# Kernel tuning notes

Measured on AMD Instinct MI355X. Metric: run time of the kernel, lower is better.

The kernel has to match this reference:

```python
import jax, jax.numpy as jnp
import numpy as np

L, D, H, B, S, V = 4, 1024, 16, 8, 512, 32000
DK = D // H          # per-head dim = 64; only head 0 is ever used (bug in source)
FF = 4 * D
EPS = 1e-3           # keras BatchNormalization default epsilon


def _bn(x, gamma, beta, mean, var):
    # inference-mode BatchNorm over last axis (keras default)
    return gamma * (x - mean) * jax.lax.rsqrt(var + EPS) + beta


def setup_inputs() -> dict:
    key = jax.random.key(0)
    keys = iter(jax.random.split(key, 40))

    def rn(shape, scale=0.02):
        return jax.random.normal(next(keys), shape, jnp.float32) * scale

    sequence = jax.random.randint(next(keys), (B, S), 0, V, dtype=jnp.int32)

    # standard sinusoidal positional encoding table [S, D]
    pos = np.arange(S)[:, None].astype(np.float32)
    i = np.arange(D)[None, :]
    angle = pos / np.power(10000.0, (2 * (i // 2)) / D).astype(np.float32)
    pes = np.where(i % 2 == 0, np.sin(angle), np.cos(angle)).astype(np.float32)

    return {
        "sequence": sequence,
        "emb": rn((V, D)),
        "pes": jnp.asarray(pes),
        # single-head attention params (head 0 only, per the source bug), stacked over layers
        "wq": rn((L, D, DK)), "bq": jnp.zeros((L, DK)),
        "wk": rn((L, D, DK)), "bk": jnp.zeros((L, DK)),
        "wv": rn((L, D, DK)), "bv": jnp.zeros((L, DK)),
        "wo": rn((L, DK, D)), "bo": jnp.zeros((L, D)),
        "att_gamma": 1.0 + rn((L, D), 0.1), "att_beta": rn((L, D), 0.1),
        "att_mean": rn((L, D), 0.1), "att_var": jnp.ones((L, D)),
        "w1": rn((L, D, FF)), "bff1": jnp.zeros((L, FF)),
        "w2": rn((L, FF, D)), "bff2": jnp.zeros((L, D)),
        "ffn_gamma": 1.0 + rn((L, D), 0.1), "ffn_beta": rn((L, D), 0.1),
        "ffn_mean": rn((L, D), 0.1), "ffn_var": jnp.ones((L, D)),
    }


def reference(sequence, emb, pes, wq, bq, wk, bk, wv, bv, wo, bo,
              att_gamma, att_beta, att_mean, att_var,
              w1, bff1, w2, bff2,
              ffn_gamma, ffn_beta, ffn_mean, ffn_var):
    # embedding + positional bug: only pes[i, 0] (a scalar per position) is added
    x = emb[sequence] + pes[:S, 0:1][None]          # [B, S, D]
    scale = 1.0 / jnp.sqrt(jnp.float32(DK))
    for l in range(L):
        q = x @ wq[l] + bq[l]                       # [B, S, DK]
        k = x @ wk[l] + bk[l]
        v = x @ wv[l] + bv[l]
        score = jnp.einsum('bqd,bkd->bqk', q, k) * scale
        head = jax.nn.softmax(score, axis=-1) @ v   # [B, S, DK]
        att = head @ wo[l] + bo[l]                  # [B, S, D]
        x = _bn(x + att, att_gamma[l], att_beta[l], att_mean[l], att_var[l])
        ffn = jax.nn.relu(x @ w1[l] + bff1[l]) @ w2[l] + bff2[l]
        x = _bn(x + ffn, ffn_gamma[l], ffn_beta[l], ffn_mean[l], ffn_var[l])
    return x
```

## Files before the change

### kernel.cpp

```cpp
#include <hip/hip_runtime.h>
#include <hip/hip_bf16.h>
#include <stdint.h>

#define L_  4
#define D_  1024
#define DK_ 64
#define B_  8
#define S_  512
#define FF_ 4096
#define M_  (B_*S_)
#define EPS_ 1e-3f
#define QKVN_ 256

typedef __bf16 bf16_t;
typedef bf16_t bf16x8 __attribute__((ext_vector_type(8)));
typedef float  f32x4  __attribute__((ext_vector_type(4)));

__device__ __forceinline__ bf16_t f2b(float f) {
    union { float f; uint32_t u; } v; v.f = f;
    uint32_t r = v.u + 0x7fff + ((v.u >> 16) & 1);
    uint16_t h = (uint16_t)(r >> 16);
    bf16_t o; __builtin_memcpy(&o, &h, 2); return o;
}

__device__ __forceinline__ void gl2lds16(const bf16_t* g, bf16_t* l) {
    __builtin_amdgcn_global_load_lds(
        (__attribute__((address_space(1))) void*)g,
        (__attribute__((address_space(3))) void*)l, 16, 0, 0);
}

__global__ void embed_kernel(const int* __restrict__ seq, const float* __restrict__ emb,
                             const float* __restrict__ pes, float* __restrict__ x,
                             bf16_t* __restrict__ xb) {
    int idx = blockIdx.x * 256 + threadIdx.x;
    int md  = idx >> 10;
    int d   = idx & (D_ - 1);
    int s   = md & (S_ - 1);
    float v = emb[(size_t)seq[md] * D_ + d] + pes[s * D_];
    x[idx] = v;
    xb[idx] = f2b(v);
}

__device__ __forceinline__ void tile_tr(const float* __restrict__ src, bf16_t* __restrict__ dst,
                                        int K, int N, int kb, int nb, float (*t)[33]) {
    int k0 = kb * 32, n0 = nb * 32;
    int c = threadIdx.x & 31, r = threadIdx.x >> 5;
    #pragma unroll
    for (int i = 0; i < 4; i++)
        t[r + i * 8][c] = src[(size_t)(k0 + r + i * 8) * N + n0 + c];
    __syncthreads();
    #pragma unroll
    for (int i = 0; i < 4; i++)
        dst[(size_t)(n0 + r + i * 8) * K + k0 + c] = f2b(t[c][r + i * 8]);
}

__global__ void prep_weights(const float* __restrict__ wq, const float* __restrict__ wk,
                             const float* __restrict__ wv, const float* __restrict__ wo,
                             const float* __restrict__ w1, const float* __restrict__ w2,
                             const float* __restrict__ bq, const float* __restrict__ bk,
                             const float* __restrict__ bv,
                             bf16_t* __restrict__ wqkvt, bf16_t* __restrict__ wot,
                             bf16_t* __restrict__ w1t, bf16_t* __restrict__ w2t,
                             float* __restrict__ bqkv) {
    __shared__ float t[32][33];
    int bid = blockIdx.x;
    if (bid < 4096) {
        tile_tr(w1, w1t, D_, FF_, bid & 31, bid >> 5, t);
    } else if (bid < 8192) {
        int rem = bid - 4096;
        tile_tr(w2, w2t, FF_, D_, rem & 127, rem >> 7, t);
    } else if (bid < 8384) {
        int rem = bid - 8192;
        int which = rem >> 6; rem &= 63;
        const float* src = which == 0 ? wq : (which == 1 ? wk : wv);
        tile_tr(src, wqkvt + (size_t)which * 64 * D_, D_, DK_, rem & 31, rem >> 5, t);
    } else if (bid < 8448) {
        int rem = bid - 8384;
        tile_tr(wo, wot, DK_, D_, rem & 1, rem >> 1, t);
    } else if (bid < 8464) {
        int rem = bid - 8448;
        bf16_t* z = wqkvt + (size_t)192 * D_ + rem * 4096;
        for (int i = threadIdx.x; i < 4096; i += 256) z[i] = (bf16_t)0.f;
    } else {
        int n = threadIdx.x;
        float v = 0.f;
        if      (n <  64) v = bq[n];
        else if (n < 128) v = bk[n - 64];
        else if (n < 192) v = bv[n - 128];
        bqkv[n] = v;
    }
}

template<int MODE>
__global__ __launch_bounds__(256)
void gemm_mfma3(const bf16_t* __restrict__ A, const bf16_t* __restrict__ Bt,
                const float* __restrict__ bias, bf16_t* __restrict__ Cb,
                const float* __restrict__ Xin, float* __restrict__ Xf, bf16_t* __restrict__ Xb,
                const float* __restrict__ g, const float* __restrict__ bb,
                const float* __restrict__ mu, const float* __restrict__ var,
                int N, int K, int kChunk, size_t strideZ) {
    __shared__ bf16_t As[128 * 64];
    __shared__ bf16_t Bs[128 * 64];
    const int tid  = threadIdx.x;
    const int w    = tid >> 6, lane = tid & 63;
    const int wm   = w >> 1,   wn   = w & 1;
    const int lm   = lane & 15, quad = lane >> 4;
    const int m0 = blockIdx.y * 128, n0 = blockIdx.x * 128;
    const int kBeg = blockIdx.z * kChunk, kEnd = kBeg + kChunk;
    const int lrow = lane >> 3;
    const int lk   = (lane & 7) ^ lrow;

    f32x4 acc[4][4];
    #pragma unroll
    for (int i = 0; i < 4; i++)
        #pragma unroll
        for (int j = 0; j < 4; j++) acc[i][j] = (f32x4){0.f, 0.f, 0.f, 0.f};

    for (int k0 = kBeg; k0 < kEnd; k0 += 64) {
        #pragma unroll
        for (int i = 0; i < 4; i++) {
            const int r0 = w * 32 + i * 8;
            gl2lds16(A  + (size_t)(m0 + r0 + lrow) * K + k0 + lk * 8, As + r0 * 64);
            gl2lds16(Bt + (size_t)(n0 + r0 + lrow) * K + k0 + lk * 8, Bs + r0 * 64);
        }
        __syncthreads();
        #pragma unroll
        for (int s = 0; s < 2; s++) {
            bf16x8 af[4], bfr[4];
            #pragma unroll
            for (int mi = 0; mi < 4; mi++) {
                const int ra = wm * 64 + mi * 16 + lm;
                af[mi] = *(const bf16x8*)(As + ra * 64 + (((s * 4 + quad) ^ (lm & 7)) * 8));
            }
            #pragma unroll
            for (int ni = 0; ni < 4; ni++) {
                const int rb = wn * 64 + ni * 16 + lm;
                bfr[ni] = *(const bf16x8*)(Bs + rb * 64 + (((s * 4 + quad) ^ (lm & 7)) * 8));
            }
            #pragma unroll
            for (int mi = 0; mi < 4; mi++)
                #pragma unroll
                for (int ni = 0; ni < 4; ni++)
                    acc[mi][ni] = __builtin_amdgcn_mfma_f32_16x16x32_bf16(
                        af[mi], bfr[ni], acc[mi][ni], 0, 0, 0);
        }
        __syncthreads();
    }

    bf16_t* Pz = (MODE == 2) ? Cb + (size_t)blockIdx.z * strideZ : Cb;

    #pragma unroll
    for (int ni = 0; ni < 4; ni++) {
        const int col = n0 + wn * 64 + ni * 16 + lm;
        float bv = 0.f, gv = 0.f, bbv = 0.f, muv = 0.f, rsv = 0.f;
        if (MODE != 2) bv = bias[col];
        if (MODE == 3) {
            gv = g[col]; bbv = bb[col]; muv = mu[col];
            rsv = rsqrtf(var[col] + EPS_);
        }
        #pragma unroll
        for (int mi = 0; mi < 4; mi++) {
            const int rbase = m0 + wm * 64 + mi * 16 + quad * 4;
            #pragma unroll
            for (int r = 0; r < 4; r++) {
                const size_t idx = (size_t)(rbase + r) * N + col;
                float v = acc[mi][ni][r] + bv;
                if (MODE == 1) Cb[idx] = f2b(fmaxf(v, 0.f));
                if (MODE == 2) Pz[idx] = f2b(v);
                if (MODE == 3) {
                    float s = Xin[idx] + v;
                    float o = gv * (s - muv) * rsv + bbv;
                    Xf[idx] = o;
                    Xb[idx] = f2b(o);
                }
            }
        }
    }
}

__global__ void qkv_reduce(const bf16_t* __restrict__ P, const float* __restrict__ bias,
                           bf16_t* __restrict__ dst) {
    int idx = blockIdx.x * 256 + threadIdx.x;
    int n = idx & (QKVN_ - 1);
    float s = bias[n];
    #pragma unroll
    for (int zz = 0; zz < 4; zz++) s += (float)P[(size_t)zz * M_ * QKVN_ + idx];
    dst[idx] = f2b(s);
}

__global__ void score_kernel(const bf16_t* __restrict__ qkv, float* __restrict__ sc, float scale) {
    int b = blockIdx.z;
    int i0 = blockIdx.y * 64, j0 = blockIdx.x * 64;
    const bf16_t* qb = qkv + (size_t)b * S_ * QKVN_;
    const bf16_t* kb = qb + 64;
    __shared__ float Qs[64][65], Ks[64][65];
    const int tid = threadIdx.y * 16 + threadIdx.x;
    #pragma unroll
    for (int t = 0; t < 16; t++) {
        int idx = tid + t * 256;
        int r = idx >> 6, c = idx & 63;
        Qs[r][c] = (float)qb[(size_t)(i0 + r) * QKVN_ + c];
        Ks[r][c] = (float)kb[(size_t)(j0 + r) * QKVN_ + c];
    }
    __syncthreads();
    float acc[4][4] = {};
    #pragma unroll 8
    for (int d = 0; d < DK_; d++) {
        float a[4], bbv[4];
        #pragma unroll
        for (int i = 0; i < 4; i++) a[i]   = Qs[threadIdx.y * 4 + i][d];
        #pragma unroll
        for (int j = 0; j < 4; j++) bbv[j] = Ks[threadIdx.x * 4 + j][d];
        #pragma unroll
        for (int i = 0; i < 4; i++)
            #pragma unroll
            for (int j = 0; j < 4; j++) acc[i][j] = fmaf(a[i], bbv[j], acc[i][j]);
    }
    float* sb = sc + (size_t)b * S_ * S_;
    #pragma unroll
    for (int i = 0; i < 4; i++)
        #pragma unroll
        for (int j = 0; j < 4; j++)
            sb[(size_t)(i0 + threadIdx.y * 4 + i) * S_ + j0 + threadIdx.x * 4 + j] = acc[i][j] * scale;
}

__global__ void softmax_kernel(float* __restrict__ sc) {
    float* p = sc + (size_t)blockIdx.x * S_;
    int tid = threadIdx.x;
    float v0 = p[tid], v1 = p[tid + 256];
    float m = fmaxf(v0, v1);
    #pragma unroll
    for (int off = 32; off > 0; off >>= 1) m = fmaxf(m, __shfl_xor(m, off, 64));
    __shared__ float wmax[4], wsum[4];
    int wid = tid >> 6, lane = tid & 63;
    if (lane == 0) wmax[wid] = m;
    __syncthreads();
    m = fmaxf(fmaxf(wmax[0], wmax[1]), fmaxf(wmax[2], wmax[3]));
    v0 = __expf(v0 - m); v1 = __expf(v1 - m);
    float s = v0 + v1;
    #pragma unroll
    for (int off = 32; off > 0; off >>= 1) s += __shfl_xor(s, off, 64);
    if (lane == 0) wsum[wid] = s;
    __syncthreads();
    float inv = 1.0f / (wsum[0] + wsum[1] + wsum[2] + wsum[3]);
    p[tid] = v0 * inv; p[tid + 256] = v1 * inv;
}

__global__ void pv_kernel(const float* __restrict__ P, const bf16_t* __restrict__ qkv,
                          float* __restrict__ Hp) {
    int b = blockIdx.z, sp = blockIdx.x;
    const float*  Pb = P + (size_t)b * S_ * S_;
    const bf16_t* Vb = qkv + (size_t)b * S_ * QKVN_ + 128;
    float* Hb = Hp + (size_t)sp * M_ * DK_ + (size_t)b * S_ * DK_;
    int m0 = blockIdx.y * 64;
    __shared__ float Ps[16][65], Vs[16][65];
    const int tid = threadIdx.y * 16 + threadIdx.x;
    float acc[4][4] = {};
    for (int k0 = sp * 128; k0 < sp * 128 + 128; k0 += 16) {
        #pragma unroll
        for (int t = 0; t < 4; t++) {
            int idx = tid + t * 256;
            int r = idx >> 4, c = idx & 15;
            Ps[c][r] = Pb[(size_t)(m0 + r) * S_ + k0 + c];
            int br = idx >> 6, bc = idx & 63;
            Vs[br][bc] = (float)Vb[(size_t)(k0 + br) * QKVN_ + bc];
        }
        __syncthreads();
        #pragma unroll
        for (int kk = 0; kk < 16; kk++) {
            float a[4], bbv[4];
            #pragma unroll
            for (int i = 0; i < 4; i++) a[i]   = Ps[kk][threadIdx.y * 4 + i];
            #pragma unroll
            for (int j = 0; j < 4; j++) bbv[j] = Vs[kk][threadIdx.x * 4 + j];
            #pragma unroll
            for (int i = 0; i < 4; i++)
                #pragma unroll
                for (int j = 0; j < 4; j++) acc[i][j] = fmaf(a[i], bbv[j], acc[i][j]);
        }
        __syncthreads();
    }
    #pragma unroll
    for (int i = 0; i < 4; i++)
        #pragma unroll
        for (int j = 0; j < 4; j++)
            Hb[(size_t)(m0 + threadIdx.y * 4 + i) * DK_ + threadIdx.x * 4 + j] = acc[i][j];
}

__global__ void pv_reduce(const float* __restrict__ Hp, bf16_t* __restrict__ hdb) {
    int idx = blockIdx.x * 256 + threadIdx.x;
    float s = Hp[idx] + Hp[(size_t)M_ * DK_ + idx]
            + Hp[2 * (size_t)M_ * DK_ + idx] + Hp[3 * (size_t)M_ * DK_ + idx];
    hdb[idx] = f2b(s);
}

__global__ void bn_residual2(const float* __restrict__ x, const bf16_t* __restrict__ p,
                             const float* __restrict__ bias,
                             const float* __restrict__ g, const float* __restrict__ b,
                             const float* __restrict__ mu, const float* __restrict__ var,
                             float* __restrict__ dst, bf16_t* __restrict__ dstb) {
    int idx = blockIdx.x * 256 + threadIdx.x;
    int d = idx & (D_ - 1);
    float r = bias[d] + (float)p[idx] + (float)p[(size_t)M_ * D_ + idx];
    float s = x[idx] + r;
    float o = g[d] * (s - mu[d]) * rsqrtf(var[d] + EPS_) + b[d];
    dst[idx] = o;
    dstb[idx] = f2b(o);
}

extern "C" void kernel_launch(void* const* d_in, const int* in_sizes, int n_in,
                              void* d_out, int out_size, void* d_ws, size_t ws_size,
                              hipStream_t stream) {
    const int*   seq = (const int*)  d_in[0];
    const float* emb = (const float*)d_in[1];
    const float* pes = (const float*)d_in[2];
    const float* wq  = (const float*)d_in[3];
    const float* bq  = (const float*)d_in[4];
    const float* wk  = (const float*)d_in[5];
    const float* bk  = (const float*)d_in[6];
    const float* wv  = (const float*)d_in[7];
    const float* bv  = (const float*)d_in[8];
    const float* wo  = (const float*)d_in[9];
    const float* bo  = (const float*)d_in[10];
    const float* ag  = (const float*)d_in[11];
    const float* ab  = (const float*)d_in[12];
    const float* am  = (const float*)d_in[13];
    const float* av  = (const float*)d_in[14];
    const float* w1  = (const float*)d_in[15];
    const float* b1  = (const float*)d_in[16];
    const float* w2  = (const float*)d_in[17];
    const float* b2  = (const float*)d_in[18];
    const float* fg  = (const float*)d_in[19];
    const float* fb  = (const float*)d_in[20];
    const float* fm  = (const float*)d_in[21];
    const float* fv  = (const float*)d_in[22];
    float* out = (float*)d_out;

    char* p = (char*)d_ws;
    auto alloc = [&](size_t bytes) { char* q = p; p += (bytes + 255) & ~(size_t)255; return q; };
    float*  X     = (float*) alloc((size_t)M_ * D_ * 4);
    bf16_t* Xb    = (bf16_t*)alloc((size_t)M_ * D_ * 2);
    bf16_t* qkvb  = (bf16_t*)alloc((size_t)M_ * QKVN_ * 2);
    float*  sc    = (float*) alloc((size_t)B_ * S_ * S_ * 4);
    bf16_t* hdb   = (bf16_t*)alloc((size_t)M_ * DK_ * 2);
    bf16_t* hb    = (bf16_t*)alloc((size_t)M_ * FF_ * 2);
    bf16_t* w1t   = (bf16_t*)alloc((size_t)FF_ * D_ * 2);
    bf16_t* w2t   = (bf16_t*)alloc((size_t)D_ * FF_ * 2);
    bf16_t* wqkvt = (bf16_t*)alloc((size_t)QKVN_ * D_ * 2);
    bf16_t* wot   = (bf16_t*)alloc((size_t)D_ * DK_ * 2);
    float*  bqkv  = (float*) alloc(QKVN_ * 4);

    dim3 blk(16, 16);
    embed_kernel<<<M_ * D_ / 256, 256, 0, stream>>>(seq, emb, pes, X, Xb);

    for (int l = 0; l < L_; l++) {
        prep_weights<<<8465, 256, 0, stream>>>(
            wq + (size_t)l * D_ * DK_, wk + (size_t)l * D_ * DK_, wv + (size_t)l * D_ * DK_,
            wo + (size_t)l * DK_ * D_, w1 + (size_t)l * D_ * FF_, w2 + (size_t)l * FF_ * D_,
            bq + l * DK_, bk + l * DK_, bv + l * DK_,
            wqkvt, wot, w1t, w2t, bqkv);

        gemm_mfma3<2><<<dim3(QKVN_ / 128, M_ / 128, 4), 256, 0, stream>>>(
            Xb, wqkvt, nullptr, (bf16_t*)out, nullptr, nullptr, nullptr,
            nullptr, nullptr, nullptr, nullptr, QKVN_, D_, D_ / 4, (size_t)M_ * QKVN_);
        qkv_reduce<<<M_ * QKVN_ / 256, 256, 0, stream>>>((const bf16_t*)out, bqkv, qkvb);

        score_kernel<<<dim3(S_ / 64, S_ / 64, B_), blk, 0, stream>>>(qkvb, sc, 0.125f);
        softmax_kernel<<<B_ * S_, 256, 0, stream>>>(sc);
        pv_kernel<<<dim3(4, S_ / 64, B_), blk, 0, stream>>>(sc, qkvb, (float*)out);
        pv_reduce<<<M_ * DK_ / 256, 256, 0, stream>>>((const float*)out, hdb);

        gemm_mfma3<3><<<dim3(D_ / 128, M_ / 128, 1), 256, 0, stream>>>(
            hdb, wot, bo + l * D_, nullptr, X, X, Xb,
            ag + l * D_, ab + l * D_, am + l * D_, av + l * D_, D_, DK_, DK_, 0);

        gemm_mfma3<1><<<dim3(FF_ / 128, M_ / 128, 1), 256, 0, stream>>>(
            Xb, w1t, b1 + l * FF_, hb, nullptr, nullptr, nullptr,
            nullptr, nullptr, nullptr, nullptr, FF_, D_, D_, 0);

        gemm_mfma3<2><<<dim3(D_ / 128, M_ / 128, 2), 256, 0, stream>>>(
            hb, w2t, nullptr, (bf16_t*)out, nullptr, nullptr, nullptr,
            nullptr, nullptr, nullptr, nullptr, D_, FF_, FF_ / 2, (size_t)M_ * D_);

        bn_residual2<<<M_ * D_ / 256, 256, 0, stream>>>(
            X, (const bf16_t*)out, b2 + l * D_,
            fg + l * D_, fb + l * D_, fm + l * D_, fv + l * D_, X, Xb);
        if (l == L_ - 1)
            hipMemcpyAsync(out, X, (size_t)M_ * D_ * 4, hipMemcpyDeviceToDevice, stream);
    }
}
```

Before: 986.3 us.

## Fuse score, softmax and PV into one MFMA attention kernel

Replaces the four-kernel scalar-FMA attention path (score, softmax, split PV, reduce) with a fused kernel. It computes QK^T with bf16 MFMA, does the softmax in registers with LDS row reductions, and multiplies P by a pre-transposed V from swizzled LDS. A small transpose kernel writes V^T so it can be staged with wide loads. This removes the fp32 score matrix round trip to global memory and several launches. The trade-offs are that probabilities are rounded to bf16 before the PV product, and the grid is only 64 blocks per layer with large LDS use.

```diff
diff --git a/kernel.cpp b/kernel.cpp
--- a/kernel.cpp
+++ b/kernel.cpp
@@ -188,110 +188,173 @@
     dst[idx] = f2b(s);
 }
 
-__global__ void score_kernel(const bf16_t* __restrict__ qkv, float* __restrict__ sc, float scale) {
-    int b = blockIdx.z;
-    int i0 = blockIdx.y * 64, j0 = blockIdx.x * 64;
-    const bf16_t* qb = qkv + (size_t)b * S_ * QKVN_;
-    const bf16_t* kb = qb + 64;
-    __shared__ float Qs[64][65], Ks[64][65];
-    const int tid = threadIdx.y * 16 + threadIdx.x;
-    #pragma unroll
-    for (int t = 0; t < 16; t++) {
-        int idx = tid + t * 256;
-        int r = idx >> 6, c = idx & 63;
-        Qs[r][c] = (float)qb[(size_t)(i0 + r) * QKVN_ + c];
-        Ks[r][c] = (float)kb[(size_t)(j0 + r) * QKVN_ + c];
+__global__ void vt_kernel(const bf16_t* __restrict__ qkv, bf16_t* __restrict__ Vt) {
+    int b = blockIdx.y, k0 = blockIdx.x * 64;
+    const bf16_t* vb = qkv + (size_t)b * S_ * QKVN_ + 128;
+    __shared__ bf16_t t[64][65];
+    int c = threadIdx.x & 63, r4 = threadIdx.x >> 6;
+    #pragma unroll
+    for (int i = 0; i < 16; i++) {
+        int k = i * 4 + r4;
+        t[c][k] = vb[(size_t)(k0 + k) * QKVN_ + c];
     }
     __syncthreads();
-    float acc[4][4] = {};
-    #pragma unroll 8
-    for (int d = 0; d < DK_; d++) {
-        float a[4], bbv[4];
-        #pragma unroll
-        for (int i = 0; i < 4; i++) a[i]   = Qs[threadIdx.y * 4 + i][d];
-        #pragma unroll
-        for (int j = 0; j < 4; j++) bbv[j] = Ks[threadIdx.x * 4 + j][d];
-        #pragma unroll
-        for (int i = 0; i < 4; i++)
-            #pragma unroll
-            for (int j = 0; j < 4; j++) acc[i][j] = fmaf(a[i], bbv[j], acc[i][j]);
-    }
-    float* sb = sc + (size_t)b * S_ * S_;
-    #pragma unroll
-    for (int i = 0; i < 4; i++)
-        #pragma unroll
-        for (int j = 0; j < 4; j++)
-            sb[(size_t)(i0 + threadIdx.y * 4 + i) * S_ + j0 + threadIdx.x * 4 + j] = acc[i][j] * scale;
-}
-
-__global__ void softmax_kernel(float* __restrict__ sc) {
-    float* p = sc + (size_t)blockIdx.x * S_;
-    int tid = threadIdx.x;
-    float v0 = p[tid], v1 = p[tid + 256];
-    float m = fmaxf(v0, v1);
-    #pragma unroll
-    for (int off = 32; off > 0; off >>= 1) m = fmaxf(m, __shfl_xor(m, off, 64));
-    __shared__ float wmax[4], wsum[4];
-    int wid = tid >> 6, lane = tid & 63;
-    if (lane == 0) wmax[wid] = m;
+    #pragma unroll
+    for (int i = 0; i < 16; i++) {
+        int d = i * 4 + r4;
+        Vt[((size_t)b * DK_ + d) * S_ + k0 + c] = t[d][c];
+    }
+}
+
+__global__ __launch_bounds__(256)
+void attn_fused(const bf16_t* __restrict__ qkv, const bf16_t* __restrict__ Vt,
+                bf16_t* __restrict__ hdb) {
+    const int b  = blockIdx.y;
+    const int i0 = blockIdx.x * 64;
+    const bf16_t* qb  = qkv + (size_t)b * S_ * QKVN_;
+    const bf16_t* kb  = qb + 64;
+    const bf16_t* vtb = Vt + (size_t)b * DK_ * S_;
+
+    __shared__ bf16_t Ps[8 * 64 * 64];
+    __shared__ bf16_t Vs[8 * 64 * 64];
+    __shared__ float  rowred[4][64];
+
+    const int tid  = threadIdx.x;
+    const int w    = tid >> 6, lane = tid & 63;
+    const int lm   = lane & 15, quad = lane >> 4;
+    const int lrow = lane >> 3;
+    const int lk   = (lane & 7) ^ lrow;
+
+    #pragma unroll
+    for (int i = 0; i < 16; i++) {
+        const int r0 = w * 16 + (i & 1) * 8;
+        const int kt = i >> 1;
+        gl2lds16(vtb + (size_t)(r0 + lrow) * S_ + kt * 64 + lk * 8,
+                 Vs + kt * 4096 + r0 * 64);
+    }
+
+    f32x4 acc[4][8];
+    #pragma unroll
+    for (int mi = 0; mi < 4; mi++)
+        #pragma unroll
+        for (int ni = 0; ni < 8; ni++) acc[mi][ni] = (f32x4){0.f, 0.f, 0.f, 0.f};
+
+    #pragma unroll
+    for (int s = 0; s < 2; s++) {
+        bf16x8 af[4], bfr[8];
+        #pragma unroll
+        for (int mi = 0; mi < 4; mi++)
+            af[mi] = *(const bf16x8*)(qb + (size_t)(i0 + mi * 16 + lm) * QKVN_ + s * 32 + quad * 8);
+        #pragma unroll
+        for (int ni = 0; ni < 8; ni++)
+            bfr[ni] = *(const bf16x8*)(kb + (size_t)(w * 128 + ni * 16 + lm) * QKVN_ + s * 32 + quad * 8);
+        #pragma unroll
+        for (int mi = 0; mi < 4; mi++)
+            #pragma unroll
+            for (int ni = 0; ni < 8; ni++)
+                acc[mi][ni] = __builtin_amdgcn_mfma_f32_16x16x32_bf16(
+                    af[mi], bfr[ni], acc[mi][ni], 0, 0, 0);
+    }
+    #pragma unroll
+    for (int mi = 0; mi < 4; mi++)
+        #pragma unroll
+        for (int ni = 0; ni < 8; ni++) acc[mi][ni] *= 0.125f;
+
+    float rmax[4][4];
+    #pragma unroll
+    for (int mi = 0; mi < 4; mi++)
+        #pragma unroll
+        for (int r = 0; r < 4; r++) {
+            float m = acc[mi][0][r];
+            #pragma unroll
+            for (int ni = 1; ni < 8; ni++) m = fmaxf(m, acc[mi][ni][r]);
+            #pragma unroll
+            for (int off = 1; off < 16; off <<= 1) m = fmaxf(m, __shfl_xor(m, off, 64));
+            rmax[mi][r] = m;
+        }
+    if (lm == 0) {
+        #pragma unroll
+        for (int mi = 0; mi < 4; mi++)
+            #pragma unroll
+            for (int r = 0; r < 4; r++)
+                rowred[w][mi * 16 + quad * 4 + r] = rmax[mi][r];
+    }
     __syncthreads();
-    m = fmaxf(fmaxf(wmax[0], wmax[1]), fmaxf(wmax[2], wmax[3]));
-    v0 = __expf(v0 - m); v1 = __expf(v1 - m);
-    float s = v0 + v1;
-    #pragma unroll
-    for (int off = 32; off > 0; off >>= 1) s += __shfl_xor(s, off, 64);
-    if (lane == 0) wsum[wid] = s;
+    float gmax[4][4];
+    #pragma unroll
+    for (int mi = 0; mi < 4; mi++)
+        #pragma unroll
+        for (int r = 0; r < 4; r++) {
+            const int row = mi * 16 + quad * 4 + r;
+            gmax[mi][r] = fmaxf(fmaxf(rowred[0][row], rowred[1][row]),
+                                fmaxf(rowred[2][row], rowred[3][row]));
+        }
     __syncthreads();
-    float inv = 1.0f / (wsum[0] + wsum[1] + wsum[2] + wsum[3]);
-    p[tid] = v0 * inv; p[tid + 256] = v1 * inv;
-}
-
-__global__ void pv_kernel(const float* __restrict__ P, const bf16_t* __restrict__ qkv,
-                          float* __restrict__ Hp) {
-    int b = blockIdx.z, sp = blockIdx.x;
-    const float*  Pb = P + (size_t)b * S_ * S_;
-    const bf16_t* Vb = qkv + (size_t)b * S_ * QKVN_ + 128;
-    float* Hb = Hp + (size_t)sp * M_ * DK_ + (size_t)b * S_ * DK_;
-    int m0 = blockIdx.y * 64;
-    __shared__ float Ps[16][65], Vs[16][65];
-    const int tid = threadIdx.y * 16 + threadIdx.x;
-    float acc[4][4] = {};
-    for (int k0 = sp * 128; k0 < sp * 128 + 128; k0 += 16) {
-        #pragma unroll
-        for (int t = 0; t < 4; t++) {
-            int idx = tid + t * 256;
-            int r = idx >> 4, c = idx & 15;
-            Ps[c][r] = Pb[(size_t)(m0 + r) * S_ + k0 + c];
-            int br = idx >> 6, bc = idx & 63;
-            Vs[br][bc] = (float)Vb[(size_t)(k0 + br) * QKVN_ + bc];
-        }
-        __syncthreads();
-        #pragma unroll
-        for (int kk = 0; kk < 16; kk++) {
-            float a[4], bbv[4];
-            #pragma unroll
-            for (int i = 0; i < 4; i++) a[i]   = Ps[kk][threadIdx.y * 4 + i];
-            #pragma unroll
-            for (int j = 0; j < 4; j++) bbv[j] = Vs[kk][threadIdx.x * 4 + j];
-            #pragma unroll
-            for (int i = 0; i < 4; i++)
-                #pragma unroll
-                for (int j = 0; j < 4; j++) acc[i][j] = fmaf(a[i], bbv[j], acc[i][j]);
-        }
-        __syncthreads();
-    }
-    #pragma unroll
-    for (int i = 0; i < 4; i++)
-        #pragma unroll
-        for (int j = 0; j < 4; j++)
-            Hb[(size_t)(m0 + threadIdx.y * 4 + i) * DK_ + threadIdx.x * 4 + j] = acc[i][j];
-}
-
-__global__ void pv_reduce(const float* __restrict__ Hp, bf16_t* __restrict__ hdb) {
-    int idx = blockIdx.x * 256 + threadIdx.x;
-    float s = Hp[idx] + Hp[(size_t)M_ * DK_ + idx]
-            + Hp[2 * (size_t)M_ * DK_ + idx] + Hp[3 * (size_t)M_ * DK_ + idx];
-    hdb[idx] = f2b(s);
+
+    float rsum[4][4];
+    #pragma unroll
+    for (int mi = 0; mi < 4; mi++)
+        #pragma unroll
+        for (int r = 0; r < 4; r++) rsum[mi][r] = 0.f;
+    #pragma unroll
+    for (int mi = 0; mi < 4; mi++) {
+        #pragma unroll
+        for (int ni = 0; ni < 8; ni++) {
+            const int key = w * 128 + ni * 16 + lm;
+            const int kt  = key >> 6;
+            const int ck  = (key >> 3) & 7;
+            #pragma unroll
+            for (int r = 0; r < 4; r++) {
+                const int m = mi * 16 + quad * 4 + r;
+                float p = __expf(acc[mi][ni][r] - gmax[mi][r]);
+                bf16_t pb = f2b(p);
+                rsum[mi][r] += (float)pb;
+                Ps[kt * 4096 + m * 64 + ((ck ^ (m & 7)) * 8) + (key & 7)] = pb;
+            }
+        }
+    }
+    #pragma unroll
+    for (int mi = 0; mi < 4; mi++)
+        #pragma unroll
+        for (int r = 0; r < 4; r++) {
+            float s = rsum[mi][r];
+            #pragma unroll
+            for (int off = 1; off < 16; off <<= 1) s += __shfl_xor(s, off, 64);
+            rsum[mi][r] = s;
+        }
+    if (lm == 0) {
+        #pragma unroll
+        for (int mi = 0; mi < 4; mi++)
+            #pragma unroll
+            for (int r = 0; r < 4; r++)
+                rowred[w][mi * 16 + quad * 4 + r] = rsum[mi][r];
+    }
+    __syncthreads();
+
+    f32x4 accO[4];
+    #pragma unroll
+    for (int ni = 0; ni < 4; ni++) accO[ni] = (f32x4){0.f, 0.f, 0.f, 0.f};
+    #pragma unroll
+    for (int ks = 0; ks < 16; ks++) {
+        const int kt = ks >> 1;
+        const int co = (ks & 1) * 4 + quad;
+        bf16x8 af = *(const bf16x8*)(Ps + kt * 4096 + (w * 16 + lm) * 64 + ((co ^ (lm & 7)) * 8));
+        #pragma unroll
+        for (int ni = 0; ni < 4; ni++) {
+            bf16x8 bfr = *(const bf16x8*)(Vs + kt * 4096 + (ni * 16 + lm) * 64 + ((co ^ (lm & 7)) * 8));
+            accO[ni] = __builtin_amdgcn_mfma_f32_16x16x32_bf16(af, bfr, accO[ni], 0, 0, 0);
+        }
+    }
+
+    #pragma unroll
+    for (int r = 0; r < 4; r++) {
+        const int row = w * 16 + quad * 4 + r;
+        const float tot = rowred[0][row] + rowred[1][row] + rowred[2][row] + rowred[3][row];
+        const float inv = 1.0f / tot;
+        #pragma unroll
+        for (int ni = 0; ni < 4; ni++)
+            hdb[(size_t)(b * S_ + i0 + row) * DK_ + ni * 16 + lm] = f2b(accO[ni][r] * inv);
+    }
 }
 
 __global__ void bn_residual2(const float* __restrict__ x, const bf16_t* __restrict__ p,
@@ -341,7 +404,7 @@
     float*  X     = (float*) alloc((size_t)M_ * D_ * 4);
     bf16_t* Xb    = (bf16_t*)alloc((size_t)M_ * D_ * 2);
     bf16_t* qkvb  = (bf16_t*)alloc((size_t)M_ * QKVN_ * 2);
-    float*  sc    = (float*) alloc((size_t)B_ * S_ * S_ * 4);
+    bf16_t* Vtb   = (bf16_t*)alloc((size_t)B_ * DK_ * S_ * 2);
     bf16_t* hdb   = (bf16_t*)alloc((size_t)M_ * DK_ * 2);
     bf16_t* hb    = (bf16_t*)alloc((size_t)M_ * FF_ * 2);
     bf16_t* w1t   = (bf16_t*)alloc((size_t)FF_ * D_ * 2);
@@ -350,7 +413,6 @@
     bf16_t* wot   = (bf16_t*)alloc((size_t)D_ * DK_ * 2);
     float*  bqkv  = (float*) alloc(QKVN_ * 4);
 
-    dim3 blk(16, 16);
     embed_kernel<<<M_ * D_ / 256, 256, 0, stream>>>(seq, emb, pes, X, Xb);
 
     for (int l = 0; l < L_; l++) {
@@ -365,10 +427,8 @@
             nullptr, nullptr, nullptr, nullptr, QKVN_, D_, D_ / 4, (size_t)M_ * QKVN_);
         qkv_reduce<<<M_ * QKVN_ / 256, 256, 0, stream>>>((const bf16_t*)out, bqkv, qkvb);
 
-        score_kernel<<<dim3(S_ / 64, S_ / 64, B_), blk, 0, stream>>>(qkvb, sc, 0.125f);
-        softmax_kernel<<<B_ * S_, 256, 0, stream>>>(sc);
-        pv_kernel<<<dim3(4, S_ / 64, B_), blk, 0, stream>>>(sc, qkvb, (float*)out);
-        pv_reduce<<<M_ * DK_ / 256, 256, 0, stream>>>((const float*)out, hdb);
+        vt_kernel<<<dim3(S_ / 64, B_), 256, 0, stream>>>(qkvb, Vtb);
+        attn_fused<<<dim3(S_ / 64, B_), 256, 0, stream>>>(qkvb, Vtb, hdb);
 
         gemm_mfma3<3><<<dim3(D_ / 128, M_ / 128, 1), 256, 0, stream>>>(
             hdb, wot, bo + l * D_, nullptr, X, X, Xb,
```

Result: faster. 919.3 us (-6.8%).
